# Kernel optimization log

Hardware: AMD Instinct MI355X
Metric: run time of the kernel (lower is better)

Reference implementation:

```python
import jax, jax.numpy as jnp
import numpy as np

N_NODES = 50000
N_EDGES = 800000
D_IN = 128
D_HID = 128
D_OUT = 128


def _gcn_layer(x, W, b, src, dst, norm):
    # dense projection then edge-weighted gather -> scatter-add at dst
    h = x @ W                                   # [N, d_out]
    msg = h[src] * norm[:, None]                # [E, d_out]
    out = jax.ops.segment_sum(msg, dst, num_segments=N_NODES)
    return out + b


def setup_inputs() -> dict:
    key = jax.random.key(0)
    k = jax.random.split(key, 8)
    x = jax.random.normal(k[0], (N_NODES, D_IN), dtype=jnp.float32)
    edge_index = jax.random.randint(k[1], (2, N_EDGES), 0, N_NODES, dtype=jnp.int64)
    edge_weight = jax.random.uniform(k[2], (N_EDGES,), dtype=jnp.float32)
    # GCNConv params (glorot-ish scale)
    s1 = 1.0 / np.sqrt(D_IN)
    s2 = 1.0 / np.sqrt(D_HID)
    W1 = jax.random.normal(k[3], (D_IN, D_HID), dtype=jnp.float32) * s1
    b1 = jnp.zeros((D_HID,), dtype=jnp.float32)
    W2 = jax.random.normal(k[4], (D_HID, D_OUT), dtype=jnp.float32) * s2
    b2 = jnp.zeros((D_OUT,), dtype=jnp.float32)
    return {"x": x, "edge_index": edge_index, "edge_weight": edge_weight,
            "W1": W1, "b1": b1, "W2": W2, "b2": b2}


def reference(x, edge_index, edge_weight, W1, b1, W2, b2):
    src, dst = edge_index[0], edge_index[1]
    # gcn_norm (add_self_loops=False): deg from scatter-add of edge_weight at dst
    deg = jax.ops.segment_sum(edge_weight, dst, num_segments=N_NODES)
    dinv = jnp.where(deg > 0, jax.lax.rsqrt(jnp.maximum(deg, 1e-30)), 0.0)
    norm = dinv[src] * edge_weight * dinv[dst]  # [E]
    h = jax.nn.relu(_gcn_layer(x, W1, b1, src, dst, norm))
    out = _gcn_layer(h, W2, b2, src, dst, norm)
    # F.dropout in eval mode (deterministic reference) is identity
    return out
```

## Files before the change

### kernel.cpp

```cpp
#include <hip/hip_runtime.h>

#define N_NODES 50000
#define N_EDGES 800000
#define D 128
#define MAXDEG 64
#define NBUCK 196
#define BUCKCAP 5120
#define EB1 391

typedef __attribute__((ext_vector_type(8))) short bf16x8;
typedef __attribute__((ext_vector_type(4))) float f32x4;

__device__ inline unsigned short f2bf(float f) {
    unsigned u = __float_as_uint(f);
    unsigned r = (u + 0x7fffu + ((u >> 16) & 1u)) >> 16;
    return (unsigned short)r;
}

__global__ __launch_bounds__(256) void k_bucket(const int* __restrict__ src,
                                                const int* __restrict__ dst,
                                                const float* __restrict__ ew,
                                                int* __restrict__ cursor,
                                                uint2* __restrict__ buck,
                                                const float* __restrict__ W1,
                                                const float* __restrict__ W2,
                                                unsigned short* __restrict__ Wt1,
                                                unsigned short* __restrict__ Wt2) {
    if (blockIdx.x >= EB1) {
        const float* W = (blockIdx.x == EB1) ? W1 : W2;
        unsigned short* Wt = (blockIdx.x == EB1) ? Wt1 : Wt2;
        for (int idx = threadIdx.x; idx < D * D; idx += 256) {
            int n = idx & 127, k = idx >> 7;
            Wt[n * D + k] = f2bf(W[k * D + n]);
        }
        return;
    }
    __shared__ int hist[NBUCK];
    __shared__ int base[NBUCK];
    for (int i = threadIdx.x; i < NBUCK; i += 256) hist[i] = 0;
    __syncthreads();
    int e0 = blockIdx.x * 2048 + threadIdx.x;
    int dl[8]; unsigned pay[8]; int bk[8]; bool val[8];
    #pragma unroll
    for (int j = 0; j < 8; ++j) {
        int e = e0 + j * 256;
        val[j] = e < N_EDGES;
        if (val[j]) {
            dl[j] = dst[e];
            int s = src[e];
            unsigned wf = min(__float2uint_rn(ew[e] * 65536.f), 65535u);
            pay[j] = ((unsigned)s << 16) | wf;
            bk[j] = dl[j] >> 8;
            atomicAdd(&hist[bk[j]], 1);
        }
    }
    __syncthreads();
    for (int i = threadIdx.x; i < NBUCK; i += 256) {
        int h = hist[i];
        base[i] = h ? atomicAdd(&cursor[i], h) : 0;
    }
    __syncthreads();
    for (int i = threadIdx.x; i < NBUCK; i += 256) hist[i] = 0;
    __syncthreads();
    #pragma unroll
    for (int j = 0; j < 8; ++j) {
        if (val[j]) {
            int slot = base[bk[j]] + atomicAdd(&hist[bk[j]], 1);
            if (slot < BUCKCAP)
                buck[(size_t)bk[j] * BUCKCAP + slot] = make_uint2(pay[j], dl[j] & 255);
        }
    }
}

__global__ __launch_bounds__(256) void k_build(const int* __restrict__ cursor,
                                               const uint2* __restrict__ buck,
                                               unsigned* __restrict__ csr,
                                               int* __restrict__ cnt,
                                               float* __restrict__ dinv) {
    __shared__ unsigned csr_loc[256 * MAXDEG];
    __shared__ int cnt_loc[256];
    __shared__ int deg_loc[256];
    int b = blockIdx.x, tid = threadIdx.x;
    cnt_loc[tid] = 0;
    deg_loc[tid] = 0;
    __syncthreads();
    int n = min(cursor[b], BUCKCAP);
    const uint2* bb = buck + (size_t)b * BUCKCAP;
    for (int i = tid; i < n; i += 256) {
        uint2 e = bb[i];
        int ln = e.y;
        int slot = atomicAdd(&cnt_loc[ln], 1);
        if (slot < MAXDEG) csr_loc[ln * MAXDEG + slot] = e.x;
        atomicAdd(&deg_loc[ln], (int)(e.x & 0xffffu));
    }
    __syncthreads();
    int node0 = b * 256;
    int nnodes = min(256, N_NODES - node0);
    uint4* g = (uint4*)(csr + (size_t)node0 * MAXDEG);
    const uint4* l = (const uint4*)csr_loc;
    int nv = nnodes * (MAXDEG / 4);
    for (int i = tid; i < nv; i += 256) g[i] = l[i];
    if (tid < nnodes) {
        int node = node0 + tid;
        cnt[node] = min(cnt_loc[tid], MAXDEG);
        float sum = (float)deg_loc[tid] * (1.f / 65536.f);
        dinv[node] = sum > 0.f ? rsqrtf(fmaxf(sum, 1e-30f)) : 0.f;
    }
}

__global__ __launch_bounds__(256) void k_gemm(const void* __restrict__ Xv,
                                              const unsigned short* __restrict__ Wt,
                                              const float* __restrict__ dinv,
                                              unsigned short* __restrict__ Yb,
                                              int xIsF32) {
    __shared__ unsigned short sX[64 * D];
    int row0 = blockIdx.x * 64;
    int nr = min(64, N_NODES - row0);
    if (xIsF32) {
        const float4* xs = (const float4*)((const float*)Xv + (size_t)row0 * D);
        int nvec = nr * (D / 4);
        for (int i = threadIdx.x; i < nvec; i += 256) {
            float4 v = xs[i];
            ushort4 o;
            o.x = f2bf(v.x); o.y = f2bf(v.y); o.z = f2bf(v.z); o.w = f2bf(v.w);
            *(ushort4*)(sX + i * 4) = o;
        }
    } else {
        const uint4* xs = (const uint4*)((const unsigned short*)Xv + (size_t)row0 * D);
        int nvec = nr * (D / 8);
        for (int i = threadIdx.x; i < nvec; i += 256)
            *(uint4*)(sX + i * 8) = xs[i];
    }
    __syncthreads();

    int wave = threadIdx.x >> 6, lane = threadIdx.x & 63;
    int m = lane & 15, quad = lane >> 4;
    f32x4 acc[8];
    #pragma unroll
    for (int i = 0; i < 8; ++i) acc[i] = (f32x4){0.f, 0.f, 0.f, 0.f};

    const unsigned short* aBase = sX + (wave * 16 + m) * D + quad * 8;
    #pragma unroll
    for (int c = 0; c < 4; ++c) {
        bf16x8 a = *(const bf16x8*)(aBase + c * 32);
        #pragma unroll
        for (int n0 = 0; n0 < 8; ++n0) {
            bf16x8 b = *(const bf16x8*)(Wt + (n0 * 16 + m) * D + c * 32 + quad * 8);
            acc[n0] = __builtin_amdgcn_mfma_f32_16x16x32_bf16(a, b, acc[n0], 0, 0, 0);
        }
    }

    float dv[4];
    #pragma unroll
    for (int i = 0; i < 4; ++i) {
        int r = row0 + wave * 16 + quad * 4 + i;
        dv[i] = dinv ? (r < N_NODES ? dinv[r] : 0.f) : 1.f;
    }

    unsigned short* sOut = sX + wave * 16 * D;
    __syncthreads();
    #pragma unroll
    for (int n0 = 0; n0 < 8; ++n0)
        #pragma unroll
        for (int i = 0; i < 4; ++i)
            sOut[(quad * 4 + i) * D + n0 * 16 + m] = f2bf(acc[n0][i] * dv[i]);
    __syncthreads();
    int rr = lane >> 2, c0 = (lane & 3) * 32;
    int grow = row0 + wave * 16 + rr;
    if (grow < N_NODES) {
        uint4* dstp = (uint4*)(Yb + (size_t)grow * D + c0);
        const uint4* srcp = (const uint4*)(sOut + rr * D + c0);
        dstp[0] = srcp[0]; dstp[1] = srcp[1]; dstp[2] = srcp[2]; dstp[3] = srcp[3];
    }
}

__global__ __launch_bounds__(256) void k_aggregate(const unsigned short* __restrict__ H,
                                                   const int* __restrict__ cnt,
                                                   const unsigned* __restrict__ csr,
                                                   const float* __restrict__ dinv,
                                                   const float* __restrict__ bias,
                                                   void* __restrict__ out,
                                                   int relu, int out_bf16) {
    int node = blockIdx.x * 4 + (threadIdx.x >> 6);
    int lane = threadIdx.x & 63;
    int g = lane >> 4;
    int fl = lane & 15;
    int end = min(cnt[node], MAXDEG);
    int nw = (end + 15) >> 4;
    const uint4* row4 = (const uint4*)(csr + (size_t)node * MAXDEG);
    uint4 c4[4];
    #pragma unroll
    for (int w = 0; w < 4; ++w)
        if (w < nw) c4[w] = row4[w * 4 + g];
    float acc[8] = {0.f, 0.f, 0.f, 0.f, 0.f, 0.f, 0.f, 0.f};
    #pragma unroll
    for (int w = 0; w < 4; ++w) {
        if (w < nw) {
            int k0 = w * 16 + g * 4;
            unsigned cs[4] = {c4[w].x, c4[w].y, c4[w].z, c4[w].w};
            #pragma unroll
            for (int j = 0; j < 4; ++j) {
                if (k0 + j < end) {
                    unsigned s = cs[j] >> 16;
                    float nm = (float)(cs[j] & 0xffffu) * (1.f / 65536.f);
                    uint4 u = *(const uint4*)(H + (size_t)s * D + fl * 8);
                    unsigned a0[4] = {u.x, u.y, u.z, u.w};
                    #pragma unroll
                    for (int q = 0; q < 4; ++q) {
                        acc[2 * q]     += __uint_as_float(a0[q] << 16) * nm;
                        acc[2 * q + 1] += __uint_as_float(a0[q] & 0xffff0000u) * nm;
                    }
                }
            }
        }
    }
    #pragma unroll
    for (int j = 0; j < 8; ++j) {
        acc[j] += __shfl_xor(acc[j], 16, 64);
        acc[j] += __shfl_xor(acc[j], 32, 64);
    }
    if (g < 2) {
        float dn = dinv[node];
        int f = fl * 8 + g * 4;
        float v[4];
        #pragma unroll
        for (int j = 0; j < 4; ++j) {
            v[j] = acc[g * 4 + j] * dn + bias[f + j];
            if (relu) v[j] = fmaxf(v[j], 0.f);
        }
        if (out_bf16) {
            ushort4 o;
            o.x = f2bf(v[0]); o.y = f2bf(v[1]); o.z = f2bf(v[2]); o.w = f2bf(v[3]);
            *(ushort4*)((unsigned short*)out + (size_t)node * D + f) = o;
        } else {
            *(float4*)((float*)out + (size_t)node * D + f) =
                make_float4(v[0], v[1], v[2], v[3]);
        }
    }
}

extern "C" void kernel_launch(void* const* d_in, const int* in_sizes, int n_in,
                              void* d_out, int out_size, void* d_ws, size_t ws_size,
                              hipStream_t stream) {
    const float* x   = (const float*)d_in[0];
    const int*   ei  = (const int*)d_in[1];
    const float* ew  = (const float*)d_in[2];
    const float* W1  = (const float*)d_in[3];
    const float* b1  = (const float*)d_in[4];
    const float* W2  = (const float*)d_in[5];
    const float* b2  = (const float*)d_in[6];
    float* out = (float*)d_out;

    const int* src = ei;
    const int* dst = ei + N_EDGES;

    char* base = (char*)d_ws;
    size_t off = 0;
    auto take = [&](size_t bytes) -> char* {
        char* p = base + off;
        off += (bytes + 255) & ~(size_t)255;
        return p;
    };
    int*      cursor = (int*)take(NBUCK * 4);
    size_t zero_bytes = off;
    float*    dinv = (float*)take(N_NODES * 4);
    int*      cnt  = (int*)take(N_NODES * 4);
    uint2*    buck = (uint2*)take((size_t)NBUCK * BUCKCAP * 8);
    unsigned* csr  = (unsigned*)take((size_t)N_NODES * MAXDEG * 4);
    unsigned short* Wt1 = (unsigned short*)take(D * D * 2);
    unsigned short* Wt2 = (unsigned short*)take(D * D * 2);
    unsigned short* h0  = (unsigned short*)take((size_t)N_NODES * D * 2);
    unsigned short* h1  = (unsigned short*)take((size_t)N_NODES * D * 2);

    hipMemsetAsync(d_ws, 0, zero_bytes, stream);

    const int GB = (N_NODES + 63) / 64;
    const int AB = N_NODES / 4;

    k_bucket<<<EB1 + 2, 256, 0, stream>>>(src, dst, ew, cursor, buck,
                                          W1, W2, Wt1, Wt2);
    k_build<<<NBUCK, 256, 0, stream>>>(cursor, buck, csr, cnt, dinv);

    k_gemm<<<GB, 256, 0, stream>>>(x, Wt1, dinv, h0, 1);
    k_aggregate<<<AB, 256, 0, stream>>>(h0, cnt, csr, dinv, b1, h1, 1, 1);

    k_gemm<<<GB, 256, 0, stream>>>(h1, Wt2, dinv, h0, 0);
    k_aggregate<<<AB, 256, 0, stream>>>(h0, cnt, csr, dinv, b2, out, 0, 0);
}
```

Measured before the change: 233.4 us.

## Fuse layer-1 aggregation with layer-2 GEMM and locally sort edge buckets

Layer-1 aggregation, bias, and ReLU are merged with the layer-2 projection into one kernel. It stages 16 aggregated rows in shared memory and multiplies them by W2 with MFMA, which removes one launch and a bf16 round trip through global memory. The bucketing kernel now handles 4096 edges per block and sorts them by bucket in shared memory before writing, so global bucket writes become contiguous. The costs are fewer, heavier blocks in the fused kernel, lower occupancy from the aggregation phase, and a block-wide scan in bucketing.

```diff
diff --git a/kernel.cpp b/kernel.cpp
--- a/kernel.cpp
+++ b/kernel.cpp
@@ -6,7 +6,8 @@
 #define MAXDEG 64
 #define NBUCK 196
 #define BUCKCAP 5120
-#define EB1 391
+#define EPB 4096
+#define NBB 196
 
 typedef __attribute__((ext_vector_type(8))) short bf16x8;
 typedef __attribute__((ext_vector_type(4))) float f32x4;
@@ -26,49 +27,65 @@
                                                 const float* __restrict__ W2,
                                                 unsigned short* __restrict__ Wt1,
                                                 unsigned short* __restrict__ Wt2) {
-    if (blockIdx.x >= EB1) {
-        const float* W = (blockIdx.x == EB1) ? W1 : W2;
-        unsigned short* Wt = (blockIdx.x == EB1) ? Wt1 : Wt2;
+    if (blockIdx.x >= NBB) {
+        const float* W = (blockIdx.x == NBB) ? W1 : W2;
+        unsigned short* Wt = (blockIdx.x == NBB) ? Wt1 : Wt2;
         for (int idx = threadIdx.x; idx < D * D; idx += 256) {
             int n = idx & 127, k = idx >> 7;
             Wt[n * D + k] = f2bf(W[k * D + n]);
         }
         return;
     }
+    __shared__ uint2 sorted[EPB];
     __shared__ int hist[NBUCK];
-    __shared__ int base[NBUCK];
-    for (int i = threadIdx.x; i < NBUCK; i += 256) hist[i] = 0;
-    __syncthreads();
-    int e0 = blockIdx.x * 2048 + threadIdx.x;
-    int dl[8]; unsigned pay[8]; int bk[8]; bool val[8];
-    #pragma unroll
-    for (int j = 0; j < 8; ++j) {
-        int e = e0 + j * 256;
-        val[j] = e < N_EDGES;
-        if (val[j]) {
-            dl[j] = dst[e];
-            int s = src[e];
+    __shared__ int scn[NBUCK];
+    __shared__ int gbase[NBUCK];
+    __shared__ int s[256];
+    int tid = threadIdx.x;
+    int e0 = blockIdx.x * EPB;
+    for (int i = tid; i < NBUCK; i += 256) hist[i] = 0;
+    __syncthreads();
+    #pragma unroll
+    for (int j = 0; j < 16; ++j) {
+        int e = e0 + j * 256 + tid;
+        if (e < N_EDGES) atomicAdd(&hist[dst[e] >> 8], 1);
+    }
+    __syncthreads();
+    int v = tid < NBUCK ? hist[tid] : 0;
+    s[tid] = v;
+    __syncthreads();
+    for (int off = 1; off < 256; off <<= 1) {
+        int u = tid >= off ? s[tid - off] : 0;
+        __syncthreads();
+        s[tid] += u;
+        __syncthreads();
+    }
+    int excl = s[tid] - v;
+    if (tid < NBUCK) {
+        scn[tid] = excl;
+        gbase[tid] = v ? atomicAdd(&cursor[tid], v) : 0;
+        hist[tid] = excl;
+    }
+    __syncthreads();
+    #pragma unroll
+    for (int j = 0; j < 16; ++j) {
+        int e = e0 + j * 256 + tid;
+        if (e < N_EDGES) {
+            int d = dst[e];
+            int sv = src[e];
             unsigned wf = min(__float2uint_rn(ew[e] * 65536.f), 65535u);
-            pay[j] = ((unsigned)s << 16) | wf;
-            bk[j] = dl[j] >> 8;
-            atomicAdd(&hist[bk[j]], 1);
-        }
-    }
-    __syncthreads();
-    for (int i = threadIdx.x; i < NBUCK; i += 256) {
-        int h = hist[i];
-        base[i] = h ? atomicAdd(&cursor[i], h) : 0;
-    }
-    __syncthreads();
-    for (int i = threadIdx.x; i < NBUCK; i += 256) hist[i] = 0;
-    __syncthreads();
-    #pragma unroll
-    for (int j = 0; j < 8; ++j) {
-        if (val[j]) {
-            int slot = base[bk[j]] + atomicAdd(&hist[bk[j]], 1);
-            if (slot < BUCKCAP)
-                buck[(size_t)bk[j] * BUCKCAP + slot] = make_uint2(pay[j], dl[j] & 255);
-        }
+            int slot = atomicAdd(&hist[d >> 8], 1);
+            sorted[slot] = make_uint2(((unsigned)sv << 16) | wf, (unsigned)d);
+        }
+    }
+    __syncthreads();
+    int total = min(EPB, N_EDGES - e0);
+    for (int i = tid; i < total; i += 256) {
+        uint2 en = sorted[i];
+        int bk = (int)(en.y >> 8);
+        int g = gbase[bk] + (i - scn[bk]);
+        if (g < BUCKCAP)
+            buck[(size_t)bk * BUCKCAP + g] = make_uint2(en.x, en.y & 255u);
     }
 }
 
@@ -108,16 +125,15 @@
     }
 }
 
-__global__ __launch_bounds__(256) void k_gemm(const void* __restrict__ Xv,
+__global__ __launch_bounds__(256) void k_gemm(const float* __restrict__ X,
                                               const unsigned short* __restrict__ Wt,
                                               const float* __restrict__ dinv,
-                                              unsigned short* __restrict__ Yb,
-                                              int xIsF32) {
+                                              unsigned short* __restrict__ Yb) {
     __shared__ unsigned short sX[64 * D];
     int row0 = blockIdx.x * 64;
     int nr = min(64, N_NODES - row0);
-    if (xIsF32) {
-        const float4* xs = (const float4*)((const float*)Xv + (size_t)row0 * D);
+    {
+        const float4* xs = (const float4*)(X + (size_t)row0 * D);
         int nvec = nr * (D / 4);
         for (int i = threadIdx.x; i < nvec; i += 256) {
             float4 v = xs[i];
@@ -125,11 +141,6 @@
             o.x = f2bf(v.x); o.y = f2bf(v.y); o.z = f2bf(v.z); o.w = f2bf(v.w);
             *(ushort4*)(sX + i * 4) = o;
         }
-    } else {
-        const uint4* xs = (const uint4*)((const unsigned short*)Xv + (size_t)row0 * D);
-        int nvec = nr * (D / 8);
-        for (int i = threadIdx.x; i < nvec; i += 256)
-            *(uint4*)(sX + i * 8) = xs[i];
     }
     __syncthreads();
 
@@ -154,7 +165,7 @@
     #pragma unroll
     for (int i = 0; i < 4; ++i) {
         int r = row0 + wave * 16 + quad * 4 + i;
-        dv[i] = dinv ? (r < N_NODES ? dinv[r] : 0.f) : 1.f;
+        dv[i] = r < N_NODES ? dinv[r] : 0.f;
     }
 
     unsigned short* sOut = sX + wave * 16 * D;
@@ -174,13 +185,101 @@
     }
 }
 
+__global__ __launch_bounds__(256) void k_agg_mm(const unsigned short* __restrict__ H,
+                                                const int* __restrict__ cnt,
+                                                const unsigned* __restrict__ csr,
+                                                const float* __restrict__ dinv,
+                                                const float* __restrict__ b1,
+                                                const unsigned short* __restrict__ Wt2,
+                                                unsigned short* __restrict__ Hb) {
+    __shared__ unsigned short sT[16 * D];
+    int tid = threadIdx.x, wave = tid >> 6, lane = tid & 63;
+    int g = lane >> 4, fl = lane & 15;
+    int nb = blockIdx.x * 16;
+
+    for (int nn = 0; nn < 4; ++nn) {
+        int node = nb + wave * 4 + nn;
+        int end = min(cnt[node], MAXDEG);
+        int nw = (end + 15) >> 4;
+        const uint4* row4 = (const uint4*)(csr + (size_t)node * MAXDEG);
+        uint4 c4[4];
+        #pragma unroll
+        for (int w = 0; w < 4; ++w)
+            if (w < nw) c4[w] = row4[w * 4 + g];
+        float acc[8] = {0.f, 0.f, 0.f, 0.f, 0.f, 0.f, 0.f, 0.f};
+        #pragma unroll
+        for (int w = 0; w < 4; ++w) {
+            if (w < nw) {
+                int k0 = w * 16 + g * 4;
+                unsigned cs[4] = {c4[w].x, c4[w].y, c4[w].z, c4[w].w};
+                #pragma unroll
+                for (int j = 0; j < 4; ++j) {
+                    if (k0 + j < end) {
+                        unsigned sv = cs[j] >> 16;
+                        float nm = (float)(cs[j] & 0xffffu) * (1.f / 65536.f);
+                        uint4 u = *(const uint4*)(H + (size_t)sv * D + fl * 8);
+                        unsigned a0[4] = {u.x, u.y, u.z, u.w};
+                        #pragma unroll
+                        for (int q = 0; q < 4; ++q) {
+                            acc[2 * q]     += __uint_as_float(a0[q] << 16) * nm;
+                            acc[2 * q + 1] += __uint_as_float(a0[q] & 0xffff0000u) * nm;
+                        }
+                    }
+                }
+            }
+        }
+        #pragma unroll
+        for (int j = 0; j < 8; ++j) {
+            acc[j] += __shfl_xor(acc[j], 16, 64);
+            acc[j] += __shfl_xor(acc[j], 32, 64);
+        }
+        if (g < 2) {
+            float dn = dinv[node];
+            int f = fl * 8 + g * 4;
+            ushort4 o;
+            o.x = f2bf(fmaxf(acc[g * 4 + 0] * dn + b1[f + 0], 0.f));
+            o.y = f2bf(fmaxf(acc[g * 4 + 1] * dn + b1[f + 1], 0.f));
+            o.z = f2bf(fmaxf(acc[g * 4 + 2] * dn + b1[f + 2], 0.f));
+            o.w = f2bf(fmaxf(acc[g * 4 + 3] * dn + b1[f + 3], 0.f));
+            *(ushort4*)(sT + (wave * 4 + nn) * D + f) = o;
+        }
+    }
+    __syncthreads();
+
+    int m = lane & 15, quad = lane >> 4;
+    f32x4 acc2[2];
+    acc2[0] = (f32x4){0.f, 0.f, 0.f, 0.f};
+    acc2[1] = (f32x4){0.f, 0.f, 0.f, 0.f};
+    #pragma unroll
+    for (int c = 0; c < 4; ++c) {
+        bf16x8 a = *(const bf16x8*)(sT + m * D + c * 32 + quad * 8);
+        #pragma unroll
+        for (int t = 0; t < 2; ++t) {
+            int n0 = wave * 2 + t;
+            bf16x8 b = *(const bf16x8*)(Wt2 + (n0 * 16 + m) * D + c * 32 + quad * 8);
+            acc2[t] = __builtin_amdgcn_mfma_f32_16x16x32_bf16(a, b, acc2[t], 0, 0, 0);
+        }
+    }
+    float dv[4];
+    #pragma unroll
+    for (int i = 0; i < 4; ++i) dv[i] = dinv[nb + quad * 4 + i];
+    __syncthreads();
+    #pragma unroll
+    for (int t = 0; t < 2; ++t)
+        #pragma unroll
+        for (int i = 0; i < 4; ++i)
+            sT[(quad * 4 + i) * D + (wave * 2 + t) * 16 + m] = f2bf(acc2[t][i] * dv[i]);
+    __syncthreads();
+    int rr = tid >> 4, cc = (tid & 15) * 8;
+    *(uint4*)(Hb + (size_t)(nb + rr) * D + cc) = *(const uint4*)(sT + rr * D + cc);
+}
+
 __global__ __launch_bounds__(256) void k_aggregate(const unsigned short* __restrict__ H,
                                                    const int* __restrict__ cnt,
                                                    const unsigned* __restrict__ csr,
                                                    const float* __restrict__ dinv,
                                                    const float* __restrict__ bias,
-                                                   void* __restrict__ out,
-                                                   int relu, int out_bf16) {
+                                                   float* __restrict__ out) {
     int node = blockIdx.x * 4 + (threadIdx.x >> 6);
     int lane = threadIdx.x & 63;
     int g = lane >> 4;
@@ -201,9 +300,9 @@
             #pragma unroll
             for (int j = 0; j < 4; ++j) {
                 if (k0 + j < end) {
-                    unsigned s = cs[j] >> 16;
+                    unsigned sv = cs[j] >> 16;
                     float nm = (float)(cs[j] & 0xffffu) * (1.f / 65536.f);
-                    uint4 u = *(const uint4*)(H + (size_t)s * D + fl * 8);
+                    uint4 u = *(const uint4*)(H + (size_t)sv * D + fl * 8);
                     unsigned a0[4] = {u.x, u.y, u.z, u.w};
                     #pragma unroll
                     for (int q = 0; q < 4; ++q) {
@@ -222,20 +321,11 @@
     if (g < 2) {
         float dn = dinv[node];
         int f = fl * 8 + g * 4;
-        float v[4];
-        #pragma unroll
-        for (int j = 0; j < 4; ++j) {
-            v[j] = acc[g * 4 + j] * dn + bias[f + j];
-            if (relu) v[j] = fmaxf(v[j], 0.f);
-        }
-        if (out_bf16) {
-            ushort4 o;
-            o.x = f2bf(v[0]); o.y = f2bf(v[1]); o.z = f2bf(v[2]); o.w = f2bf(v[3]);
-            *(ushort4*)((unsigned short*)out + (size_t)node * D + f) = o;
-        } else {
-            *(float4*)((float*)out + (size_t)node * D + f) =
-                make_float4(v[0], v[1], v[2], v[3]);
-        }
+        *(float4*)(out + (size_t)node * D + f) =
+            make_float4(acc[g * 4 + 0] * dn + bias[f + 0],
+                        acc[g * 4 + 1] * dn + bias[f + 1],
+                        acc[g * 4 + 2] * dn + bias[f + 2],
+                        acc[g * 4 + 3] * dn + bias[f + 3]);
     }
 }
 
@@ -270,20 +360,19 @@
     unsigned short* Wt1 = (unsigned short*)take(D * D * 2);
     unsigned short* Wt2 = (unsigned short*)take(D * D * 2);
     unsigned short* h0  = (unsigned short*)take((size_t)N_NODES * D * 2);
-    unsigned short* h1  = (unsigned short*)take((size_t)N_NODES * D * 2);
+    unsigned short* hb  = (unsigned short*)take((size_t)N_NODES * D * 2);
 
     hipMemsetAsync(d_ws, 0, zero_bytes, stream);
 
     const int GB = (N_NODES + 63) / 64;
+    const int FB = N_NODES / 16;
     const int AB = N_NODES / 4;
 
-    k_bucket<<<EB1 + 2, 256, 0, stream>>>(src, dst, ew, cursor, buck,
+    k_bucket<<<NBB + 2, 256, 0, stream>>>(src, dst, ew, cursor, buck,
                                           W1, W2, Wt1, Wt2);
     k_build<<<NBUCK, 256, 0, stream>>>(cursor, buck, csr, cnt, dinv);
 
-    k_gemm<<<GB, 256, 0, stream>>>(x, Wt1, dinv, h0, 1);
-    k_aggregate<<<AB, 256, 0, stream>>>(h0, cnt, csr, dinv, b1, h1, 1, 1);
-
-    k_gemm<<<GB, 256, 0, stream>>>(h1, Wt2, dinv, h0, 0);
-    k_aggregate<<<AB, 256, 0, stream>>>(h0, cnt, csr, dinv, b2, out, 0, 0);
-}
+    k_gemm<<<GB, 256, 0, stream>>>(x, Wt1, dinv, h0);
+    k_agg_mm<<<FB, 256, 0, stream>>>(h0, cnt, csr, dinv, b1, Wt2, hb);
+    k_aggregate<<<AB, 256, 0, stream>>>(hb, cnt, csr, dinv, b2, out);
+}
```

After: 214.1 us. 1.09x faster.
